# Performance work log

Measured on AMD Instinct MI355X. Metric: run time of the kernel, lower is better.

## Reference

```python
import jax, jax.numpy as jnp
import numpy as np

EPS = 1e-12  # torch F.normalize default eps
COMMITMENT_COST = 0.25

def l2_normalize(v, axis=-1):
    # matches torch.nn.functional.normalize(p=2): v / max(||v||, eps)
    n = jnp.linalg.norm(v, axis=axis, keepdims=True)
    return v / jnp.maximum(n, EPS)

def setup_inputs() -> dict:
    key = jax.random.key(0)
    k1, k2 = jax.random.split(key)
    N, D, K = 262144, 64, 1024
    x = jax.random.normal(k1, (N, D), dtype=jnp.float32)
    emb_weight = jax.random.normal(k2, (K, D), dtype=jnp.float32)
    return {"x": x, "emb_weight": emb_weight}

def reference(x, emb_weight):
    # x: [N, D] latents, emb_weight: [K, D] codebook
    xn = l2_normalize(x, axis=-1)                      # F.normalize(x, dim=-1)
    wn = l2_normalize(emb_weight, axis=-1)             # normalized codebook rows
    d2 = (jnp.sum(xn * xn, axis=-1, keepdims=True)
          + jnp.sum(wn * wn, axis=1)
          - 2.0 * jnp.matmul(xn, wn.T))                # [N, K]
    encoding_indices = jnp.argmin(d2, axis=1)          # [N]
    # quantize: normalize(embeddings(idx)) == wn[idx]
    quantized = wn[encoding_indices]                   # [N, D]
    q_latent_loss = jnp.mean((quantized - jax.lax.stop_gradient(xn)) ** 2)
    e_latent_loss = jnp.mean((xn - jax.lax.stop_gradient(quantized)) ** 2)
    loss = q_latent_loss + COMMITMENT_COST * e_latent_loss
    # straight-through estimator
    quantized_st = xn + jax.lax.stop_gradient(quantized - xn)
    return quantized_st, loss, encoding_indices
```

## Files before the change

### kernel.cpp

```cpp
#include <hip/hip_runtime.h>
#include <math.h>

#define N_ROWS 262144
#define DIM 64
#define K_CODES 1024
#define EPSF 1e-12f
#define NTILES 64
#define ROWS_PER_BLOCK 128
#define ROWS_PER_WAVE 32

typedef _Float16 f16x8 __attribute__((ext_vector_type(8)));
typedef float f32x4 __attribute__((ext_vector_type(4)));


__global__ __launch_bounds__(64) void prep_codebook(
    const float* __restrict__ w, float* __restrict__ wn, float* __restrict__ sw,
    _Float16* __restrict__ wf)
{
    int k = blockIdx.x;
    int d = threadIdx.x;
    float v = w[k * DIM + d];
    float sq = v * v;
    #pragma unroll
    for (int off = 32; off; off >>= 1) sq += __shfl_xor(sq, off, 64);
    float n = fmaxf(sqrtf(sq), EPSF);
    float o = v / n;
    wn[k * DIM + d] = o;
    float s2 = o * o;
    #pragma unroll
    for (int off = 32; off; off >>= 1) s2 += __shfl_xor(s2, off, 64);
    if (d == 0) sw[k] = s2;

    _Float16 hi = (_Float16)o;
    _Float16 lo = (_Float16)(o - (float)hi);
    int t = k >> 4, nn = k & 15, s = d >> 5, g = (d >> 3) & 3, i = d & 7;
    size_t base = (size_t)t * 2048 + (size_t)s * 512 + (size_t)(g * 16 + nn) * 8 + i;
    wf[base] = hi;
    wf[base + 1024] = lo;
}

__global__ __launch_bounds__(256) void vq_main_kernel(
    const float* __restrict__ x,
    const float* __restrict__ wn,
    const float* __restrict__ sw,
    const _Float16* __restrict__ wf,
    float* __restrict__ out_q,
    float* __restrict__ out_idx,
    float* __restrict__ partial)
{
    __shared__ int   idx_lds[ROWS_PER_BLOCK];
    __shared__ float n_lds[ROWS_PER_BLOCK];
    __shared__ float red[4];

    const int tid  = threadIdx.x;
    const int w    = tid >> 6;
    const int lane = tid & 63;
    const int nidx = lane & 15;
    const int g    = lane >> 4;

    const int block_row0 = blockIdx.x * ROWS_PER_BLOCK;
    const int wave_row0  = block_row0 + w * ROWS_PER_WAVE;

    f16x8 ah[2][2], al[2][2];
    #pragma unroll
    for (int rt = 0; rt < 2; ++rt) {
        const int row = wave_row0 + rt * 16 + nidx;
        float xv[2][8];
        #pragma unroll
        for (int s = 0; s < 2; ++s) {
            const float4* p = (const float4*)(x + (size_t)row * DIM + s * 32 + g * 8);
            float4 q0 = p[0], q1 = p[1];
            xv[s][0] = q0.x; xv[s][1] = q0.y; xv[s][2] = q0.z; xv[s][3] = q0.w;
            xv[s][4] = q1.x; xv[s][5] = q1.y; xv[s][6] = q1.z; xv[s][7] = q1.w;
        }
        float ss = 0.f;
        #pragma unroll
        for (int s = 0; s < 2; ++s)
            #pragma unroll
            for (int e = 0; e < 8; ++e) ss += xv[s][e] * xv[s][e];
        ss += __shfl_xor(ss, 16, 64);
        ss += __shfl_xor(ss, 32, 64);
        float nrm = fmaxf(sqrtf(ss), EPSF);
        if (g == 0) n_lds[w * ROWS_PER_WAVE + rt * 16 + nidx] = nrm;
        #pragma unroll
        for (int s = 0; s < 2; ++s)
            #pragma unroll
            for (int e = 0; e < 8; ++e) {
                float v = xv[s][e] / nrm;
                _Float16 hi = (_Float16)v;
                ah[rt][s][e] = hi;
                al[rt][s][e] = (_Float16)(v - (float)hi);
            }
    }

    float best[2][4];
    int   bidx[2][4];
    #pragma unroll
    for (int rt = 0; rt < 2; ++rt)
        #pragma unroll
        for (int r = 0; r < 4; ++r) { best[rt][r] = 3.4e38f; bidx[rt][r] = 0; }

    for (int t = 0; t < NTILES; ++t) {
        const _Float16* bp = wf + (size_t)t * 2048 + (size_t)lane * 8;
        f16x8 bh0 = *(const f16x8*)(bp);
        f16x8 bh1 = *(const f16x8*)(bp + 512);
        f16x8 bl0 = *(const f16x8*)(bp + 1024);
        f16x8 bl1 = *(const f16x8*)(bp + 1536);
        float sval = sw[t * 16 + nidx];

        f32x4 acc0 = {0.f, 0.f, 0.f, 0.f};
        f32x4 acc1 = {0.f, 0.f, 0.f, 0.f};
        acc0 = __builtin_amdgcn_mfma_f32_16x16x32_f16(ah[0][0], bh0, acc0, 0, 0, 0);
        acc1 = __builtin_amdgcn_mfma_f32_16x16x32_f16(ah[1][0], bh0, acc1, 0, 0, 0);
        acc0 = __builtin_amdgcn_mfma_f32_16x16x32_f16(ah[0][1], bh1, acc0, 0, 0, 0);
        acc1 = __builtin_amdgcn_mfma_f32_16x16x32_f16(ah[1][1], bh1, acc1, 0, 0, 0);
        acc0 = __builtin_amdgcn_mfma_f32_16x16x32_f16(ah[0][0], bl0, acc0, 0, 0, 0);
        acc1 = __builtin_amdgcn_mfma_f32_16x16x32_f16(ah[1][0], bl0, acc1, 0, 0, 0);
        acc0 = __builtin_amdgcn_mfma_f32_16x16x32_f16(ah[0][1], bl1, acc0, 0, 0, 0);
        acc1 = __builtin_amdgcn_mfma_f32_16x16x32_f16(ah[1][1], bl1, acc1, 0, 0, 0);
        acc0 = __builtin_amdgcn_mfma_f32_16x16x32_f16(al[0][0], bh0, acc0, 0, 0, 0);
        acc1 = __builtin_amdgcn_mfma_f32_16x16x32_f16(al[1][0], bh0, acc1, 0, 0, 0);
        acc0 = __builtin_amdgcn_mfma_f32_16x16x32_f16(al[0][1], bh1, acc0, 0, 0, 0);
        acc1 = __builtin_amdgcn_mfma_f32_16x16x32_f16(al[1][1], bh1, acc1, 0, 0, 0);

        const int colbase = t * 16 + nidx;
        #pragma unroll
        for (int r = 0; r < 4; ++r) {
            float s0 = fmaf(-2.f, acc0[r], sval);
            if (s0 < best[0][r]) { best[0][r] = s0; bidx[0][r] = colbase; }
            float s1 = fmaf(-2.f, acc1[r], sval);
            if (s1 < best[1][r]) { best[1][r] = s1; bidx[1][r] = colbase; }
        }
    }

    #pragma unroll
    for (int rt = 0; rt < 2; ++rt)
        #pragma unroll
        for (int r = 0; r < 4; ++r) {
            float b = best[rt][r];
            int   i0 = bidx[rt][r];
            #pragma unroll
            for (int off = 1; off <= 8; off <<= 1) {
                float ob = __shfl_xor(b, off, 64);
                int   oi = __shfl_xor(i0, off, 64);
                if (ob < b || (ob == b && oi < i0)) { b = ob; i0 = oi; }
            }
            best[rt][r] = b;
            bidx[rt][r] = i0;
        }
    if (nidx == 0) {
        #pragma unroll
        for (int rt = 0; rt < 2; ++rt)
            #pragma unroll
            for (int r = 0; r < 4; ++r)
                idx_lds[w * ROWS_PER_WAVE + rt * 16 + g * 4 + r] = bidx[rt][r];
    }
    __syncthreads();

    const int lr   = tid >> 1;
    const int grow = block_row0 + lr;
    const int d0   = (tid & 1) * 32;
    const int ci   = idx_lds[lr];
    const float nrm = n_lds[lr];
    const float4* xp = (const float4*)(x  + (size_t)grow * DIM + d0);
    const float4* qp = (const float4*)(wn + (size_t)ci   * DIM + d0);
    float4* op = (float4*)(out_q + (size_t)grow * DIM + d0);
    float ls = 0.f;
    #pragma unroll
    for (int i = 0; i < 8; ++i) {
        float4 qv = qp[i];
        float4 xv = xp[i];
        float e0 = qv.x - xv.x / nrm;
        float e1 = qv.y - xv.y / nrm;
        float e2 = qv.z - xv.z / nrm;
        float e3 = qv.w - xv.w / nrm;
        ls += e0 * e0 + e1 * e1 + e2 * e2 + e3 * e3;
        op[i] = qv;
    }
    if (!(tid & 1)) out_idx[grow] = (float)ci;

    float s = ls;
    #pragma unroll
    for (int off = 32; off; off >>= 1) s += __shfl_xor(s, off, 64);
    if (lane == 0) red[w] = s;
    __syncthreads();
    if (tid == 0) partial[blockIdx.x] = (red[0] + red[1]) + (red[2] + red[3]);
}

__global__ __launch_bounds__(256) void finalize_kernel(
    const float* __restrict__ partial, float* __restrict__ loss_out)
{
    __shared__ float red[4];
    int t = threadIdx.x;
    float s = 0.f;
    #pragma unroll
    for (int i = 0; i < 8; ++i) s += partial[t * 8 + i];
    #pragma unroll
    for (int off = 32; off; off >>= 1) s += __shfl_xor(s, off, 64);
    if ((t & 63) == 0) red[t >> 6] = s;
    __syncthreads();
    if (t == 0)
        *loss_out = 1.25f * (((red[0] + red[1]) + (red[2] + red[3]))
                             / (float)((size_t)N_ROWS * DIM));
}

extern "C" void kernel_launch(void* const* d_in, const int* in_sizes, int n_in,
                              void* d_out, int out_size, void* d_ws, size_t ws_size,
                              hipStream_t stream) {
    const float* x = (const float*)d_in[0];
    const float* w = (const float*)d_in[1];
    float* out = (float*)d_out;
    float* ws = (float*)d_ws;

    float* wn      = ws;
    float* sw      = wn + (size_t)K_CODES * DIM;
    float* partial = sw + K_CODES;
    _Float16* wf   = (_Float16*)(partial + 2048);

    float* out_q    = out;
    float* out_loss = out + (size_t)N_ROWS * DIM;
    float* out_idx  = out_loss + 1;

    prep_codebook<<<K_CODES, 64, 0, stream>>>(w, wn, sw, wf);
    vq_main_kernel<<<N_ROWS / ROWS_PER_BLOCK, 256, 0, stream>>>(
        x, wn, sw, wf, out_q, out_idx, partial);
    finalize_kernel<<<1, 256, 0, stream>>>(partial, out_loss);
}
```

Baseline: 141.5 us.

## Switch to 32x32 MFMA tiles with LDS double-buffered codebook staging

Replaces the 16x16x32 MFMA loop, which loaded codebook fragments straight from global memory, with 32x32x16 MFMAs over 32-code tiles. Codebook tiles are staged into a double-buffered LDS array with register prefetch two tiles ahead. The -0.5*||w||^2 bias is folded into the accumulator init so the argmin becomes an argmax, and division by the norm is replaced with a reciprocal multiply. This adds a __syncthreads per tile and more LDS use in exchange for fewer global loads and less epilogue arithmetic. Occupancy is hinted at 3 blocks per CU.

```diff
diff --git a/kernel.cpp b/kernel.cpp
--- a/kernel.cpp
+++ b/kernel.cpp
@@ -4,18 +4,17 @@
 #define N_ROWS 262144
 #define DIM 64
 #define K_CODES 1024
+#define NT 32
+#define ROWS_PER_BLOCK 128
 #define EPSF 1e-12f
-#define NTILES 64
-#define ROWS_PER_BLOCK 128
-#define ROWS_PER_WAVE 32
 
 typedef _Float16 f16x8 __attribute__((ext_vector_type(8)));
-typedef float f32x4 __attribute__((ext_vector_type(4)));
+typedef float f32x16 __attribute__((ext_vector_type(16)));
 
 
 __global__ __launch_bounds__(64) void prep_codebook(
-    const float* __restrict__ w, float* __restrict__ wn, float* __restrict__ sw,
-    _Float16* __restrict__ wf)
+    const float* __restrict__ w, float* __restrict__ wn,
+    float* __restrict__ msw, _Float16* __restrict__ wf)
 {
     int k = blockIdx.x;
     int d = threadIdx.x;
@@ -29,151 +28,169 @@
     float s2 = o * o;
     #pragma unroll
     for (int off = 32; off; off >>= 1) s2 += __shfl_xor(s2, off, 64);
-    if (d == 0) sw[k] = s2;
+    if (d == 0) msw[k] = -0.5f * s2;
 
     _Float16 hi = (_Float16)o;
     _Float16 lo = (_Float16)(o - (float)hi);
-    int t = k >> 4, nn = k & 15, s = d >> 5, g = (d >> 3) & 3, i = d & 7;
-    size_t base = (size_t)t * 2048 + (size_t)s * 512 + (size_t)(g * 16 + nn) * 8 + i;
+    int t = k >> 5, nn = k & 31, s = d >> 4, g = (d >> 3) & 1, i = d & 7;
+    size_t base = (size_t)t * 4096 + (size_t)s * 512 + (size_t)(g * 32 + nn) * 8 + i;
     wf[base] = hi;
-    wf[base + 1024] = lo;
-}
-
-__global__ __launch_bounds__(256) void vq_main_kernel(
+    wf[base + 2048] = lo;
+}
+
+#define BODY(T, CW0, CW1, NL0, NL1)                                           \
+  {                                                                           \
+    const int cur = (T) & 1;                                                  \
+    const _Float16* bp = &bbuf[cur][lane * 8];                                \
+    f16x8 bh0 = *(const f16x8*)(bp);                                          \
+    f16x8 bh1 = *(const f16x8*)(bp + 512);                                    \
+    f16x8 bh2 = *(const f16x8*)(bp + 1024);                                   \
+    f16x8 bh3 = *(const f16x8*)(bp + 1536);                                   \
+    f16x8 bl0 = *(const f16x8*)(bp + 2048);                                   \
+    f16x8 bl1 = *(const f16x8*)(bp + 2560);                                   \
+    f16x8 bl2 = *(const f16x8*)(bp + 3072);                                   \
+    f16x8 bl3 = *(const f16x8*)(bp + 3584);                                   \
+    float mval = msw_lds[(T) * 32 + col];                                     \
+    if ((T) + 1 < NT) {                                                       \
+      *(f16x8*)&bbuf[cur ^ 1][tid * 16] = CW0;                                \
+      *(f16x8*)&bbuf[cur ^ 1][tid * 16 + 8] = CW1;                            \
+    }                                                                         \
+    if ((T) + 2 < NT) {                                                       \
+      NL0 = wf8[((T) + 2) * 512 + tid * 2];                                   \
+      NL1 = wf8[((T) + 2) * 512 + tid * 2 + 1];                               \
+    }                                                                         \
+    f32x16 acc;                                                               \
+    _Pragma("unroll")                                                         \
+    for (int e = 0; e < 16; ++e) acc[e] = mval;                               \
+    acc = __builtin_amdgcn_mfma_f32_32x32x16_f16(ah[0], bh0, acc, 0, 0, 0);   \
+    acc = __builtin_amdgcn_mfma_f32_32x32x16_f16(ah[1], bh1, acc, 0, 0, 0);   \
+    acc = __builtin_amdgcn_mfma_f32_32x32x16_f16(ah[2], bh2, acc, 0, 0, 0);   \
+    acc = __builtin_amdgcn_mfma_f32_32x32x16_f16(ah[3], bh3, acc, 0, 0, 0);   \
+    acc = __builtin_amdgcn_mfma_f32_32x32x16_f16(ah[0], bl0, acc, 0, 0, 0);   \
+    acc = __builtin_amdgcn_mfma_f32_32x32x16_f16(ah[1], bl1, acc, 0, 0, 0);   \
+    acc = __builtin_amdgcn_mfma_f32_32x32x16_f16(ah[2], bl2, acc, 0, 0, 0);   \
+    acc = __builtin_amdgcn_mfma_f32_32x32x16_f16(ah[3], bl3, acc, 0, 0, 0);   \
+    acc = __builtin_amdgcn_mfma_f32_32x32x16_f16(al[0], bh0, acc, 0, 0, 0);   \
+    acc = __builtin_amdgcn_mfma_f32_32x32x16_f16(al[1], bh1, acc, 0, 0, 0);   \
+    acc = __builtin_amdgcn_mfma_f32_32x32x16_f16(al[2], bh2, acc, 0, 0, 0);   \
+    acc = __builtin_amdgcn_mfma_f32_32x32x16_f16(al[3], bh3, acc, 0, 0, 0);   \
+    _Pragma("unroll")                                                         \
+    for (int e = 0; e < 16; ++e)                                              \
+      if (acc[e] > best[e]) { best[e] = acc[e]; bt[e] = (T); }                \
+    __syncthreads();                                                          \
+  }
+
+__global__ __launch_bounds__(256, 3) void vq_main_kernel(
     const float* __restrict__ x,
     const float* __restrict__ wn,
-    const float* __restrict__ sw,
+    const float* __restrict__ msw,
     const _Float16* __restrict__ wf,
     float* __restrict__ out_q,
     float* __restrict__ out_idx,
     float* __restrict__ partial)
 {
-    __shared__ int   idx_lds[ROWS_PER_BLOCK];
-    __shared__ float n_lds[ROWS_PER_BLOCK];
+    __shared__ _Float16 bbuf[2][4096];
+    __shared__ float msw_lds[K_CODES];
+    __shared__ int idx_lds[ROWS_PER_BLOCK];
+    __shared__ float inv_lds[ROWS_PER_BLOCK];
     __shared__ float red[4];
 
-    const int tid  = threadIdx.x;
-    const int w    = tid >> 6;
+    const int tid = threadIdx.x;
+    const int wv = tid >> 6;
     const int lane = tid & 63;
-    const int nidx = lane & 15;
-    const int g    = lane >> 4;
-
+    const int col = lane & 31;
+    const int g = lane >> 5;
     const int block_row0 = blockIdx.x * ROWS_PER_BLOCK;
-    const int wave_row0  = block_row0 + w * ROWS_PER_WAVE;
-
-    f16x8 ah[2][2], al[2][2];
-    #pragma unroll
-    for (int rt = 0; rt < 2; ++rt) {
-        const int row = wave_row0 + rt * 16 + nidx;
-        float xv[2][8];
-        #pragma unroll
-        for (int s = 0; s < 2; ++s) {
-            const float4* p = (const float4*)(x + (size_t)row * DIM + s * 32 + g * 8);
-            float4 q0 = p[0], q1 = p[1];
+
+    f16x8 ah[4], al[4];
+    {
+        const int arow = block_row0 + wv * 32 + col;
+        const float* xrow = x + (size_t)arow * DIM + g * 8;
+        float xv[4][8];
+        #pragma unroll
+        for (int s = 0; s < 4; ++s) {
+            float4 q0 = *(const float4*)(xrow + s * 16);
+            float4 q1 = *(const float4*)(xrow + s * 16 + 4);
             xv[s][0] = q0.x; xv[s][1] = q0.y; xv[s][2] = q0.z; xv[s][3] = q0.w;
             xv[s][4] = q1.x; xv[s][5] = q1.y; xv[s][6] = q1.z; xv[s][7] = q1.w;
         }
         float ss = 0.f;
         #pragma unroll
-        for (int s = 0; s < 2; ++s)
+        for (int s = 0; s < 4; ++s)
             #pragma unroll
-            for (int e = 0; e < 8; ++e) ss += xv[s][e] * xv[s][e];
-        ss += __shfl_xor(ss, 16, 64);
+            for (int i = 0; i < 8; ++i) ss += xv[s][i] * xv[s][i];
         ss += __shfl_xor(ss, 32, 64);
         float nrm = fmaxf(sqrtf(ss), EPSF);
-        if (g == 0) n_lds[w * ROWS_PER_WAVE + rt * 16 + nidx] = nrm;
-        #pragma unroll
-        for (int s = 0; s < 2; ++s)
+        float inv = 1.0f / nrm;
+        if (g == 0) inv_lds[wv * 32 + col] = inv;
+        #pragma unroll
+        for (int s = 0; s < 4; ++s)
             #pragma unroll
-            for (int e = 0; e < 8; ++e) {
-                float v = xv[s][e] / nrm;
+            for (int i = 0; i < 8; ++i) {
+                float v = xv[s][i] * inv;
                 _Float16 hi = (_Float16)v;
-                ah[rt][s][e] = hi;
-                al[rt][s][e] = (_Float16)(v - (float)hi);
+                ah[s][i] = hi;
+                al[s][i] = (_Float16)(v - (float)hi);
             }
     }
 
-    float best[2][4];
-    int   bidx[2][4];
-    #pragma unroll
-    for (int rt = 0; rt < 2; ++rt)
-        #pragma unroll
-        for (int r = 0; r < 4; ++r) { best[rt][r] = 3.4e38f; bidx[rt][r] = 0; }
-
-    for (int t = 0; t < NTILES; ++t) {
-        const _Float16* bp = wf + (size_t)t * 2048 + (size_t)lane * 8;
-        f16x8 bh0 = *(const f16x8*)(bp);
-        f16x8 bh1 = *(const f16x8*)(bp + 512);
-        f16x8 bl0 = *(const f16x8*)(bp + 1024);
-        f16x8 bl1 = *(const f16x8*)(bp + 1536);
-        float sval = sw[t * 16 + nidx];
-
-        f32x4 acc0 = {0.f, 0.f, 0.f, 0.f};
-        f32x4 acc1 = {0.f, 0.f, 0.f, 0.f};
-        acc0 = __builtin_amdgcn_mfma_f32_16x16x32_f16(ah[0][0], bh0, acc0, 0, 0, 0);
-        acc1 = __builtin_amdgcn_mfma_f32_16x16x32_f16(ah[1][0], bh0, acc1, 0, 0, 0);
-        acc0 = __builtin_amdgcn_mfma_f32_16x16x32_f16(ah[0][1], bh1, acc0, 0, 0, 0);
-        acc1 = __builtin_amdgcn_mfma_f32_16x16x32_f16(ah[1][1], bh1, acc1, 0, 0, 0);
-        acc0 = __builtin_amdgcn_mfma_f32_16x16x32_f16(ah[0][0], bl0, acc0, 0, 0, 0);
-        acc1 = __builtin_amdgcn_mfma_f32_16x16x32_f16(ah[1][0], bl0, acc1, 0, 0, 0);
-        acc0 = __builtin_amdgcn_mfma_f32_16x16x32_f16(ah[0][1], bl1, acc0, 0, 0, 0);
-        acc1 = __builtin_amdgcn_mfma_f32_16x16x32_f16(ah[1][1], bl1, acc1, 0, 0, 0);
-        acc0 = __builtin_amdgcn_mfma_f32_16x16x32_f16(al[0][0], bh0, acc0, 0, 0, 0);
-        acc1 = __builtin_amdgcn_mfma_f32_16x16x32_f16(al[1][0], bh0, acc1, 0, 0, 0);
-        acc0 = __builtin_amdgcn_mfma_f32_16x16x32_f16(al[0][1], bh1, acc0, 0, 0, 0);
-        acc1 = __builtin_amdgcn_mfma_f32_16x16x32_f16(al[1][1], bh1, acc1, 0, 0, 0);
-
-        const int colbase = t * 16 + nidx;
-        #pragma unroll
-        for (int r = 0; r < 4; ++r) {
-            float s0 = fmaf(-2.f, acc0[r], sval);
-            if (s0 < best[0][r]) { best[0][r] = s0; bidx[0][r] = colbase; }
-            float s1 = fmaf(-2.f, acc1[r], sval);
-            if (s1 < best[1][r]) { best[1][r] = s1; bidx[1][r] = colbase; }
+    {
+        float4 mv = *(const float4*)(msw + tid * 4);
+        *(float4*)&msw_lds[tid * 4] = mv;
+    }
+
+    const f16x8* wf8 = (const f16x8*)wf;
+    f16x8 sA0, sA1, sB0, sB1;
+    sB0 = wf8[tid * 2];
+    sB1 = wf8[tid * 2 + 1];
+    *(f16x8*)&bbuf[0][tid * 16] = sB0;
+    *(f16x8*)&bbuf[0][tid * 16 + 8] = sB1;
+    sA0 = wf8[512 + tid * 2];
+    sA1 = wf8[512 + tid * 2 + 1];
+    __syncthreads();
+
+    float best[16];
+    int bt[16];
+    #pragma unroll
+    for (int e = 0; e < 16; ++e) { best[e] = -3.4e38f; bt[e] = 0; }
+
+    for (int tt = 0; tt < NT; tt += 2) {
+        BODY(tt, sA0, sA1, sB0, sB1)
+        BODY(tt + 1, sB0, sB1, sA0, sA1)
+    }
+
+    #pragma unroll
+    for (int e = 0; e < 16; ++e) {
+        float b = best[e];
+        int bi = bt[e] * 32 + col;
+        #pragma unroll
+        for (int off = 1; off <= 16; off <<= 1) {
+            float ob = __shfl_xor(b, off, 64);
+            int oi = __shfl_xor(bi, off, 64);
+            if (ob > b || (ob == b && oi < bi)) { b = ob; bi = oi; }
         }
-    }
-
-    #pragma unroll
-    for (int rt = 0; rt < 2; ++rt)
-        #pragma unroll
-        for (int r = 0; r < 4; ++r) {
-            float b = best[rt][r];
-            int   i0 = bidx[rt][r];
-            #pragma unroll
-            for (int off = 1; off <= 8; off <<= 1) {
-                float ob = __shfl_xor(b, off, 64);
-                int   oi = __shfl_xor(i0, off, 64);
-                if (ob < b || (ob == b && oi < i0)) { b = ob; i0 = oi; }
-            }
-            best[rt][r] = b;
-            bidx[rt][r] = i0;
-        }
-    if (nidx == 0) {
-        #pragma unroll
-        for (int rt = 0; rt < 2; ++rt)
-            #pragma unroll
-            for (int r = 0; r < 4; ++r)
-                idx_lds[w * ROWS_PER_WAVE + rt * 16 + g * 4 + r] = bidx[rt][r];
-    }
-    __syncthreads();
-
-    const int lr   = tid >> 1;
+        if (col == 0)
+            idx_lds[wv * 32 + (e & 3) + 8 * (e >> 2) + 4 * g] = bi;
+    }
+    __syncthreads();
+
+    const int lr = tid >> 1;
     const int grow = block_row0 + lr;
-    const int d0   = (tid & 1) * 32;
-    const int ci   = idx_lds[lr];
-    const float nrm = n_lds[lr];
-    const float4* xp = (const float4*)(x  + (size_t)grow * DIM + d0);
-    const float4* qp = (const float4*)(wn + (size_t)ci   * DIM + d0);
+    const int d0 = (tid & 1) * 32;
+    const int ci = idx_lds[lr];
+    const float invn = inv_lds[lr];
+    const float4* xp = (const float4*)(x + (size_t)grow * DIM + d0);
+    const float4* qp = (const float4*)(wn + (size_t)ci * DIM + d0);
     float4* op = (float4*)(out_q + (size_t)grow * DIM + d0);
     float ls = 0.f;
     #pragma unroll
     for (int i = 0; i < 8; ++i) {
         float4 qv = qp[i];
-        float4 xv = xp[i];
-        float e0 = qv.x - xv.x / nrm;
-        float e1 = qv.y - xv.y / nrm;
-        float e2 = qv.z - xv.z / nrm;
-        float e3 = qv.w - xv.w / nrm;
+        float4 xv4 = xp[i];
+        float e0 = qv.x - xv4.x * invn;
+        float e1 = qv.y - xv4.y * invn;
+        float e2 = qv.z - xv4.z * invn;
+        float e3 = qv.w - xv4.w * invn;
         ls += e0 * e0 + e1 * e1 + e2 * e2 + e3 * e3;
         op[i] = qv;
     }
@@ -182,7 +199,7 @@
     float s = ls;
     #pragma unroll
     for (int off = 32; off; off >>= 1) s += __shfl_xor(s, off, 64);
-    if (lane == 0) red[w] = s;
+    if (lane == 0) red[wv] = s;
     __syncthreads();
     if (tid == 0) partial[blockIdx.x] = (red[0] + red[1]) + (red[2] + red[3]);
 }
@@ -213,16 +230,16 @@
     float* ws = (float*)d_ws;
 
     float* wn      = ws;
-    float* sw      = wn + (size_t)K_CODES * DIM;
-    float* partial = sw + K_CODES;
+    float* msw     = wn + (size_t)K_CODES * DIM;
+    float* partial = msw + K_CODES;
     _Float16* wf   = (_Float16*)(partial + 2048);
 
     float* out_q    = out;
     float* out_loss = out + (size_t)N_ROWS * DIM;
     float* out_idx  = out_loss + 1;
 
-    prep_codebook<<<K_CODES, 64, 0, stream>>>(w, wn, sw, wf);
+    prep_codebook<<<K_CODES, 64, 0, stream>>>(w, wn, msw, wf);
     vq_main_kernel<<<N_ROWS / ROWS_PER_BLOCK, 256, 0, stream>>>(
-        x, wn, sw, wf, out_q, out_idx, partial);
+        x, wn, msw, wf, out_q, out_idx, partial);
     finalize_kernel<<<1, 256, 0, stream>>>(partial, out_loss);
 }
```

After: 136.3 us. 1.04x faster.
